# Performance work log

Measured on AMD Instinct MI355X. Metric: run time of the kernel, lower is better.

Reference implementation:

```python
import jax, jax.numpy as jnp
import numpy as np

B, N, D, H, DK, DI = 64, 256, 1024, 8, 64, 2048
NEG = -1e9
SCALE = 1.0 / np.sqrt(DK).astype(np.float32)


def _ln(x, s, b, eps=1e-5):
    m = jnp.mean(x, axis=-1, keepdims=True)
    v = jnp.var(x, axis=-1, keepdims=True)
    return (x - m) * jax.lax.rsqrt(v + eps) * s + b


def _glat_basic(x, mask, npm, wq, wk, wv, wo, bo, ls1, lb1, w1, b1, w2, b2, ls2, lb2):
    # mask: [B,1,N,N] bool, True = blocked
    b, n, d = x.shape
    q = (x @ wq).reshape(b, n, H, DK).transpose(0, 2, 1, 3)  # [B,H,N,DK]
    k = (x @ wk).reshape(b, n, H, DK).transpose(0, 2, 1, 3)
    v = (x @ wv).reshape(b, n, H, DK).transpose(0, 2, 1, 3)
    scores = jnp.einsum('bhqd,bhkd->bhqk', q, k) * SCALE
    scores = jnp.where(mask, NEG, scores)
    attn = jax.nn.softmax(scores, axis=-1)
    out = jnp.einsum('bhqk,bhkd->bhqd', attn, v)
    out = out.transpose(0, 2, 1, 3).reshape(b, n, H * DK)
    out = out @ wo + bo
    out = _ln(out + x, ls1, lb1)           # attn residual + layernorm
    out = out * npm                         # non_pad_mask
    h = jax.nn.relu(out @ w1 + b1) @ w2 + b2
    out2 = _ln(h + out, ls2, lb2) * npm     # FFN residual + layernorm + mask
    return out2


def setup_inputs():
    key = jax.random.key(0)
    ks = jax.random.split(key, 40)
    p = lambda i, shape: jax.random.normal(ks[i], shape, jnp.float32) * 0.02
    inp = {
        'x': jax.random.normal(ks[0], (B, N, D), jnp.float32),
        'adj': jax.random.randint(ks[1], (B, N, N), 0, 2).astype(jnp.int32),
        'non_pad_mask': jnp.ones((B, N, 1), jnp.float32),
        'slf_attn_mask': jnp.zeros((B, N, N), jnp.int32),
    }
    i = 2
    for t in ('g', 'l'):
        inp[f'wq_{t}'] = p(i, (D, H * DK)); i += 1
        inp[f'wk_{t}'] = p(i, (D, H * DK)); i += 1
        inp[f'wv_{t}'] = p(i, (D, H * DK)); i += 1
        inp[f'wo_{t}'] = p(i, (H * DK, D)); i += 1
        inp[f'bo_{t}'] = jnp.zeros((D,), jnp.float32)
        inp[f'ln1s_{t}'] = jnp.ones((D,), jnp.float32)
        inp[f'ln1b_{t}'] = jnp.zeros((D,), jnp.float32)
        inp[f'w1_{t}'] = p(i, (D, DI)); i += 1
        inp[f'b1_{t}'] = jnp.zeros((DI,), jnp.float32)
        inp[f'w2_{t}'] = p(i, (DI, D)); i += 1
        inp[f'b2_{t}'] = jnp.zeros((D,), jnp.float32)
        inp[f'ln2s_{t}'] = jnp.ones((D,), jnp.float32)
        inp[f'ln2b_{t}'] = jnp.zeros((D,), jnp.float32)
    inp['fc_w'] = p(i, (2 * D, D)); i += 1
    inp['fc_b'] = jnp.zeros((D,), jnp.float32)
    return inp


def reference(x, adj, non_pad_mask, slf_attn_mask,
              wq_g, wk_g, wv_g, wo_g, bo_g, ln1s_g, ln1b_g, w1_g, b1_g, w2_g, b2_g, ln2s_g, ln2b_g,
              wq_l, wk_l, wv_l, wo_l, bo_l, ln1s_l, ln1b_l, w1_l, b1_l, w2_l, b2_l, ln2s_l, ln2b_l,
              fc_w, fc_b):
    pad_mask = (slf_attn_mask[:, None, :, :] != 0)            # [B,1,N,N]
    local_mask = pad_mask | (adj[:, None, :, :] == 0)         # local: only attend along edges
    x_g = _glat_basic(x, pad_mask, non_pad_mask,
                      wq_g, wk_g, wv_g, wo_g, bo_g, ln1s_g, ln1b_g,
                      w1_g, b1_g, w2_g, b2_g, ln2s_g, ln2b_g)
    x_l = _glat_basic(x, local_mask, non_pad_mask,
                      wq_l, wk_l, wv_l, wo_l, bo_l, ln1s_l, ln1b_l,
                      w1_l, b1_l, w2_l, b2_l, ln2s_l, ln2b_l)
    out = jnp.concatenate([x_g, x_l], axis=-1) @ fc_w + fc_b
    return out
```

## Files before the change

### kernel.cpp

```cpp
#include <hip/hip_runtime.h>


typedef unsigned short u16;
typedef unsigned long long u64;
typedef __bf16 bf16_t;
typedef bf16_t bf16x8 __attribute__((ext_vector_type(8)));
typedef float  f32x4  __attribute__((ext_vector_type(4)));
typedef u16    u16x8  __attribute__((ext_vector_type(8)));
typedef u16    u16x4  __attribute__((ext_vector_type(4)));

__device__ __forceinline__ float bf2f(u16 u){
  union { unsigned int i; float f; } c; c.i = ((unsigned int)u) << 16; return c.f;
}
__device__ __forceinline__ u16 f2bf(float f){
  union { float f; unsigned int u; } c; c.f = f;
  unsigned int u = c.u;
  unsigned int r = (u + 0x7fffu + ((u >> 16) & 1u)) >> 16;
  return (u16)r;
}

__device__ __forceinline__ void gl16(const u16* g, u16* l){
  __builtin_amdgcn_global_load_lds(
      (const __attribute__((address_space(1))) void*)g,
      (__attribute__((address_space(3))) void*)l, 16, 0, 0);
}

__global__ __launch_bounds__(256) void zero_out(float* out, int n){
  for (int i = blockIdx.x * 256 + threadIdx.x; i < n; i += 256 * 4096) out[i] = 0.f;
}

__global__ __launch_bounds__(256) void cvt_bf16(
    const float* __restrict__ in, u16* __restrict__ out)
{
  const size_t i = ((size_t)blockIdx.x * 256 + threadIdx.x) * 8;
  f32x4 a = *(const f32x4*)&in[i];
  f32x4 b = *(const f32x4*)&in[i + 4];
  u16x8 o;
  #pragma unroll
  for (int j = 0; j < 4; ++j){ o[j] = f2bf(a[j]); o[4+j] = f2bf(b[j]); }
  *(u16x8*)&out[i] = o;
}

__global__ __launch_bounds__(256) void transpose_w(
    const float* __restrict__ src, u16* __restrict__ dst, int K, int N, int dstOff)
{
  __shared__ u16 tile[32][33];
  const int bk = blockIdx.x * 32, bn = blockIdx.y * 32;
  const int t = threadIdx.x;
  const int r = t >> 5, c = t & 31;
  #pragma unroll
  for (int p = 0; p < 4; ++p)
    tile[r + p*8][c] = f2bf(src[(size_t)(bk + r + p*8) * N + bn + c]);
  __syncthreads();
  #pragma unroll
  for (int p = 0; p < 4; ++p)
    dst[(size_t)(dstOff + bn + r + p*8) * K + bk + c] = tile[c][r + p*8];
}

__global__ __launch_bounds__(256) void transpose_qkv6(
    const float* s0, const float* s1, const float* s2,
    const float* s3, const float* s4, const float* s5,
    u16* __restrict__ dst0, u16* __restrict__ dst1)
{
  __shared__ u16 tile[32][33];
  const int z = blockIdx.z;
  const float* src = z == 0 ? s0 : z == 1 ? s1 : z == 2 ? s2
                   : z == 3 ? s3 : z == 4 ? s4 : s5;
  u16* dst = (z < 3 ? dst0 : dst1);
  const int dstOff = (z % 3) * 512;
  const int K = 1024, N = 512;
  const int bk = blockIdx.x * 32, bn = blockIdx.y * 32;
  const int t = threadIdx.x;
  const int r = t >> 5, c = t & 31;
  #pragma unroll
  for (int p = 0; p < 4; ++p)
    tile[r + p*8][c] = f2bf(src[(size_t)(bk + r + p*8) * N + bn + c]);
  __syncthreads();
  #pragma unroll
  for (int p = 0; p < 4; ++p)
    dst[(size_t)(dstOff + bn + r + p*8) * K + bk + c] = tile[c][r + p*8];
}

__global__ __launch_bounds__(256) void transpose_wo2(
    const float* s0, const float* s1, u16* __restrict__ dst0, u16* __restrict__ dst1)
{
  __shared__ u16 tile[32][33];
  const float* src = blockIdx.z == 0 ? s0 : s1;
  u16* dst = blockIdx.z == 0 ? dst0 : dst1;
  const int K = 512, N = 1024;
  const int bk = blockIdx.x * 32, bn = blockIdx.y * 32;
  const int t = threadIdx.x;
  const int r = t >> 5, c = t & 31;
  #pragma unroll
  for (int p = 0; p < 4; ++p)
    tile[r + p*8][c] = f2bf(src[(size_t)(bk + r + p*8) * N + bn + c]);
  __syncthreads();
  #pragma unroll
  for (int p = 0; p < 4; ++p)
    dst[(size_t)(bn + r + p*8) * K + bk + c] = tile[c][r + p*8];
}

template<int RELU, int OF32, int ACC, int OUT2>
__global__ __launch_bounds__(512, 1) void gemm256(
    const u16* __restrict__ A0, const u16* __restrict__ A1,
    int Astride, int ksplit,
    const u16* __restrict__ BT, int Bld, int M, int N, int K,
    const float* __restrict__ bias, void* __restrict__ outv, int out_ld,
    u16* __restrict__ out2v, int ncut)
{
  __shared__ u16 lds[2*32768];
  const int tid  = threadIdx.x;
  const int lane = tid & 63;
  const int wid  = tid >> 6;
  const int wm = wid >> 2, wn = wid & 3;
  const int l15 = lane & 15, l4 = lane >> 4;
  const int m0 = blockIdx.x * 256, n0 = blockIdx.y * 256;

  f32x4 acc[8][4];
  #pragma unroll
  for (int i = 0; i < 8; ++i)
    #pragma unroll
    for (int j = 0; j < 4; ++j)
      acc[i][j] = (f32x4){0.f, 0.f, 0.f, 0.f};

  const int s0 = tid, s1 = tid + 512;
  const int r0 = s0 >> 3, g0 = (s0 & 7) ^ (r0 & 7);
  const int r1 = s1 >> 3, g1 = (s1 & 7) ^ (r1 & 7);

  const int nt = K >> 6;

  auto stageA = [&](int kt, int h, int buf){
    const int kb = kt * 64;
    const u16* Ab = A0; int kl = kb;
    if (kb >= ksplit){ Ab = A1; kl = kb - ksplit; }
    u16* dst = &lds[buf*32768 + h*8192];
    gl16(&Ab[(size_t)(m0 + h*128 + r0) * Astride + kl + g0*8], &dst[s0*8]);
    gl16(&Ab[(size_t)(m0 + h*128 + r1) * Astride + kl + g1*8], &dst[s1*8]);
  };
  auto stageB = [&](int kt, int h, int buf){
    const int kb = kt * 64;
    u16* dst = &lds[buf*32768 + 16384 + h*8192];
    gl16(&BT[(size_t)(n0 + h*128 + r0) * Bld + kb + g0*8], &dst[s0*8]);
    gl16(&BT[(size_t)(n0 + h*128 + r1) * Bld + kb + g1*8], &dst[s1*8]);
  };
  auto lda = [&](int i, int kc, int buf) -> bf16x8 {
    const int r = wm*128 + i*16 + l15;
    const int c = (kc*4 + l4) ^ (r & 7);
    return *(const bf16x8*)&lds[buf*32768 + r*64 + c*8];
  };
  auto ldb = [&](int j, int kc, int buf) -> bf16x8 {
    const int r = wn*64 + j*16 + l15;
    const int c = (kc*4 + l4) ^ (r & 7);
    return *(const bf16x8*)&lds[buf*32768 + 16384 + r*64 + c*8];
  };

  stageA(0, 0, 0); stageA(0, 1, 0); stageB(0, 0, 0); stageB(0, 1, 0);

  for (int t = 0; t < nt; ++t){
    const int buf = t & 1, nbuf = buf ^ 1;
    const bool pf = (t + 1 < nt);
    if (pf){
      stageA(t+1, 0, nbuf);
      asm volatile("s_waitcnt vmcnt(2)" ::: "memory");
    } else {
      asm volatile("s_waitcnt vmcnt(0)" ::: "memory");
    }
    __builtin_amdgcn_sched_barrier(0);
    __builtin_amdgcn_s_barrier();
    __builtin_amdgcn_sched_barrier(0);

    bf16x8 a_[4][2], b_[2][2];
    #pragma unroll
    for (int i = 0; i < 4; ++i){ a_[i][0] = lda(i, 0, buf); a_[i][1] = lda(i, 1, buf); }
    #pragma unroll
    for (int j = 0; j < 2; ++j){ b_[j][0] = ldb(j, 0, buf); b_[j][1] = ldb(j, 1, buf); }
    if (pf) stageA(t+1, 1, nbuf);
    __builtin_amdgcn_s_setprio(1);
    #pragma unroll
    for (int i = 0; i < 4; ++i)
      #pragma unroll
      for (int j = 0; j < 2; ++j){
        acc[i][j] = __builtin_amdgcn_mfma_f32_16x16x32_bf16(a_[i][0], b_[j][0], acc[i][j], 0,0,0);
        acc[i][j] = __builtin_amdgcn_mfma_f32_16x16x32_bf16(a_[i][1], b_[j][1], acc[i][j], 0,0,0);
      }
    __builtin_amdgcn_s_setprio(0);
    #pragma unroll
    for (int j = 0; j < 2; ++j){ b_[j][0] = ldb(2+j, 0, buf); b_[j][1] = ldb(2+j, 1, buf); }
    if (pf) stageB(t+1, 0, nbuf);
    __builtin_amdgcn_s_setprio(1);
    #pragma unroll
    for (int i = 0; i < 4; ++i)
      #pragma unroll
      for (int j = 0; j < 2; ++j){
        acc[i][2+j] = __builtin_amdgcn_mfma_f32_16x16x32_bf16(a_[i][0], b_[j][0], acc[i][2+j], 0,0,0);
        acc[i][2+j] = __builtin_amdgcn_mfma_f32_16x16x32_bf16(a_[i][1], b_[j][1], acc[i][2+j], 0,0,0);
      }
    __builtin_amdgcn_s_setprio(0);
    #pragma unroll
    for (int i = 0; i < 4; ++i){ a_[i][0] = lda(4+i, 0, buf); a_[i][1] = lda(4+i, 1, buf); }
    if (pf) stageB(t+1, 1, nbuf);
    __builtin_amdgcn_s_setprio(1);
    #pragma unroll
    for (int i = 0; i < 4; ++i)
      #pragma unroll
      for (int j = 0; j < 2; ++j){
        acc[4+i][2+j] = __builtin_amdgcn_mfma_f32_16x16x32_bf16(a_[i][0], b_[j][0], acc[4+i][2+j], 0,0,0);
        acc[4+i][2+j] = __builtin_amdgcn_mfma_f32_16x16x32_bf16(a_[i][1], b_[j][1], acc[4+i][2+j], 0,0,0);
      }
    __builtin_amdgcn_s_setprio(0);
    #pragma unroll
    for (int j = 0; j < 2; ++j){ b_[j][0] = ldb(j, 0, buf); b_[j][1] = ldb(j, 1, buf); }
    __builtin_amdgcn_s_setprio(1);
    #pragma unroll
    for (int i = 0; i < 4; ++i)
      #pragma unroll
      for (int j = 0; j < 2; ++j){
        acc[4+i][j] = __builtin_amdgcn_mfma_f32_16x16x32_bf16(a_[i][0], b_[j][0], acc[4+i][j], 0,0,0);
        acc[4+i][j] = __builtin_amdgcn_mfma_f32_16x16x32_bf16(a_[i][1], b_[j][1], acc[4+i][j], 0,0,0);
      }
    __builtin_amdgcn_s_setprio(0);

    __builtin_amdgcn_sched_barrier(0);
    __builtin_amdgcn_s_barrier();
    __builtin_amdgcn_sched_barrier(0);
  }

  u16* outp = (u16*)outv;
  int cadj = 0;
  if (OUT2 && n0 >= ncut){ outp = out2v; cadj = ncut; }
  const int rb = m0 + wm*128 + l4*4;
  const int cb = n0 + wn*64 + l15;
  #pragma unroll
  for (int i = 0; i < 8; ++i){
    #pragma unroll
    for (int j = 0; j < 4; ++j){
      const int col = cb + j*16;
      const float badd = bias ? bias[col] : 0.f;
      #pragma unroll
      for (int r = 0; r < 4; ++r){
        const int row = rb + i*16 + r;
        float y = acc[i][j][r] + badd;
        if (RELU) y = y > 0.f ? y : 0.f;
        if (OF32){
          float* po = &((float*)outv)[(size_t)row * out_ld + col];
          if (ACC) y += *po;
          *po = y;
        } else {
          u16* po = &outp[(size_t)row * out_ld + col - cadj];
          if (ACC) y += bf2f(*po);
          *po = f2bf(y);
        }
      }
    }
  }
}

__global__ __launch_bounds__(256) void mask_pack(
    const int* __restrict__ slf, const int* __restrict__ adj,
    u64* __restrict__ mb_g, u64* __restrict__ mb_l)
{
  const int idx  = blockIdx.x * 4 + (threadIdx.x >> 6);
  const int lane = threadIdx.x & 63;
  const size_t mi = (size_t)(idx >> 2) * 256 + (size_t)(idx & 3) * 64 + lane;
  const bool g = slf[mi] != 0;
  const bool l = g || (adj[mi] == 0);
  const u64 bg = __ballot(g);
  const u64 bl = __ballot(l);
  if (lane == 0){ mb_g[idx] = bg; mb_l[idx] = bl; }
}

__global__ __launch_bounds__(256) void attn_mfma(
    const u16* __restrict__ qkv0, const u16* __restrict__ qkv1,
    const u64* __restrict__ mb0, const u64* __restrict__ mb1,
    u16* __restrict__ out0, u16* __restrict__ out1)
{
  __shared__ u16 kbuf[64*64];
  __shared__ u16 vtbuf[64*64];
  __shared__ u16 pbuf[4][32*64];

  const int L  = blockIdx.y;
  const u16* qkv = L ? qkv1 : qkv0;
  const u64* mb  = L ? mb1  : mb0;
  u16*       out = L ? out1 : out0;

  const int b  = blockIdx.x >> 4;
  const int h  = (blockIdx.x >> 1) & 7;
  const int qt = blockIdx.x & 1;
  const int t  = threadIdx.x;
  const int w  = t >> 6, lane = t & 63;
  const int l15 = lane & 15, l4 = lane >> 4;

  bf16x8 qf[2][2];
  {
    const int rbase = b*256 + qt*128 + w*32;
    #pragma unroll
    for (int i = 0; i < 2; ++i)
      #pragma unroll
      for (int kc = 0; kc < 2; ++kc)
        qf[i][kc] = *(const bf16x8*)&qkv[(size_t)(rbase + i*16 + l15)*1536 + h*64 + kc*32 + l4*8];
  }

  f32x4 acc_o[2][4];
  float m_[2][4], l_[2][4];
  #pragma unroll
  for (int i = 0; i < 2; ++i){
    #pragma unroll
    for (int j = 0; j < 4; ++j) acc_o[i][j] = (f32x4){0.f,0.f,0.f,0.f};
    #pragma unroll
    for (int r = 0; r < 4; ++r){ m_[i][r] = -1e30f; l_[i][r] = 0.f; }
  }

  for (int c = 0; c < 4; ++c){
    __syncthreads();
    {
      const int kr = t >> 2, dg = (t & 3) * 16;
      const size_t rbase = (size_t)(b*256 + c*64 + kr)*1536 + h*64 + dg;
      u16x8 k0 = *(const u16x8*)&qkv[rbase + 512];
      u16x8 k1 = *(const u16x8*)&qkv[rbase + 512 + 8];
      u16x8 v0 = *(const u16x8*)&qkv[rbase + 1024];
      u16x8 v1 = *(const u16x8*)&qkv[rbase + 1024 + 8];
      const int sw = (kr & 7) << 3;
      *(u16x8*)&kbuf[kr*64 + (dg ^ sw)]       = k0;
      *(u16x8*)&kbuf[kr*64 + ((dg + 8) ^ sw)] = k1;
      #pragma unroll
      for (int e = 0; e < 8; ++e){
        const int d0 = dg + e, d1 = dg + 8 + e;
        vtbuf[d0*64 + (kr ^ ((d0 & 7) << 3))] = v0[e];
        vtbuf[d1*64 + (kr ^ ((d1 & 7) << 3))] = v1[e];
      }
    }
    __syncthreads();

    bf16x8 kfr[4][2];
    #pragma unroll
    for (int jb = 0; jb < 4; ++jb){
      const int key = jb*16 + l15;
      const int sw = (key & 7) << 3;
      #pragma unroll
      for (int kc = 0; kc < 2; ++kc)
        kfr[jb][kc] = *(const bf16x8*)&kbuf[key*64 + ((kc*32 + l4*8) ^ sw)];
    }
    f32x4 s_[2][4];
    #pragma unroll
    for (int i = 0; i < 2; ++i)
      #pragma unroll
      for (int jb = 0; jb < 4; ++jb){
        f32x4 a = (f32x4){0.f,0.f,0.f,0.f};
        a = __builtin_amdgcn_mfma_f32_16x16x32_bf16(qf[i][0], kfr[jb][0], a, 0,0,0);
        a = __builtin_amdgcn_mfma_f32_16x16x32_bf16(qf[i][1], kfr[jb][1], a, 0,0,0);
        s_[i][jb] = a;
      }

    #pragma unroll
    for (int i = 0; i < 2; ++i)
      #pragma unroll
      for (int r = 0; r < 4; ++r){
        const int qrow = qt*128 + w*32 + i*16 + l4*4 + r;
        const u64 bits = mb[((size_t)b*256 + qrow)*4 + c];
        #pragma unroll
        for (int jb = 0; jb < 4; ++jb){
          float xv = s_[i][jb][r] * 0.125f;
          if ((bits >> (jb*16 + l15)) & 1ull) xv = -1e9f;
          s_[i][jb][r] = xv;
        }
      }
    float mxs[2][4];
    bool okall = true;
    #pragma unroll
    for (int i = 0; i < 2; ++i)
      #pragma unroll
      for (int r = 0; r < 4; ++r){
        float mx = fmaxf(fmaxf(s_[i][0][r], s_[i][1][r]),
                         fmaxf(s_[i][2][r], s_[i][3][r]));
        #pragma unroll
        for (int d = 1; d < 16; d <<= 1)
          mx = fmaxf(mx, __shfl_xor(mx, d, 64));
        mxs[i][r] = mx;
        okall = okall && (mx <= m_[i][r] + 8.f);
      }
    if (__all(okall)){
      #pragma unroll
      for (int i = 0; i < 2; ++i)
        #pragma unroll
        for (int r = 0; r < 4; ++r){
          const int prow = i*16 + l4*4 + r;
          const int swp = (prow & 7) << 3;
          float ps = 0.f;
          #pragma unroll
          for (int jb = 0; jb < 4; ++jb){
            const float p = __expf(s_[i][jb][r] - m_[i][r]);
            ps += p;
            pbuf[w][prow*64 + ((jb*16 + l15) ^ swp)] = f2bf(p);
          }
          #pragma unroll
          for (int d = 1; d < 16; d <<= 1)
            ps += __shfl_xor(ps, d, 64);
          l_[i][r] += ps;
        }
    } else {
      #pragma unroll
      for (int i = 0; i < 2; ++i)
        #pragma unroll
        for (int r = 0; r < 4; ++r){
          const int prow = i*16 + l4*4 + r;
          const float mnew = fmaxf(m_[i][r], mxs[i][r]);
          const float corr = __expf(m_[i][r] - mnew);
          m_[i][r] = mnew;
          float ps = 0.f;
          const int swp = (prow & 7) << 3;
          #pragma unroll
          for (int jb = 0; jb < 4; ++jb){
            const float p = __expf(s_[i][jb][r] - mnew);
            ps += p;
            pbuf[w][prow*64 + ((jb*16 + l15) ^ swp)] = f2bf(p);
          }
          #pragma unroll
          for (int d = 1; d < 16; d <<= 1)
            ps += __shfl_xor(ps, d, 64);
          l_[i][r] = l_[i][r] * corr + ps;
          #pragma unroll
          for (int j2 = 0; j2 < 4; ++j2) acc_o[i][j2][r] *= corr;
        }
    }

    bf16x8 vfr[4][2];
    #pragma unroll
    for (int j2 = 0; j2 < 4; ++j2){
      const int dim = j2*16 + l15;
      const int sw = (dim & 7) << 3;
      #pragma unroll
      for (int kc = 0; kc < 2; ++kc)
        vfr[j2][kc] = *(const bf16x8*)&vtbuf[dim*64 + ((kc*32 + l4*8) ^ sw)];
    }
    #pragma unroll
    for (int i = 0; i < 2; ++i){
      const int prow = i*16 + l15;
      const int swp = (prow & 7) << 3;
      bf16x8 pa0 = *(const bf16x8*)&pbuf[w][prow*64 + ((l4*8) ^ swp)];
      bf16x8 pa1 = *(const bf16x8*)&pbuf[w][prow*64 + ((32 + l4*8) ^ swp)];
      #pragma unroll
      for (int j2 = 0; j2 < 4; ++j2){
        acc_o[i][j2] = __builtin_amdgcn_mfma_f32_16x16x32_bf16(pa0, vfr[j2][0], acc_o[i][j2], 0,0,0);
        acc_o[i][j2] = __builtin_amdgcn_mfma_f32_16x16x32_bf16(pa1, vfr[j2][1], acc_o[i][j2], 0,0,0);
      }
    }
  }

  #pragma unroll
  for (int i = 0; i < 2; ++i){
    #pragma unroll
    for (int r = 0; r < 4; ++r){
      const int qrow = qt*128 + w*32 + i*16 + l4*4 + r;
      const float inv = 1.f / l_[i][r];
      const size_t ob = ((size_t)b*256 + qrow)*512 + h*64;
      #pragma unroll
      for (int j2 = 0; j2 < 4; ++j2)
        out[ob + j2*16 + l15] = f2bf(acc_o[i][j2][r] * inv);
    }
  }
}

template<int RF32>
__global__ __launch_bounds__(256) void ln_fused(
    const u16* a, const void* __restrict__ res,
    const float* __restrict__ sc, const float* __restrict__ bs,
    const float* __restrict__ npm, u16* out)
{
  const int w = threadIdx.x >> 6, lane = threadIdx.x & 63;
  const int row = blockIdx.x * 4 + w;
  const size_t bse = (size_t)row * 1024 + lane * 16;

  u16x8 av0 = *(const u16x8*)&a[bse];
  u16x8 av1 = *(const u16x8*)&a[bse + 8];
  float rv[16];
  if (RF32){
    const float* rp = (const float*)res + bse;
    #pragma unroll
    for (int j = 0; j < 16; j += 4){
      f32x4 q = *(const f32x4*)&rp[j];
      rv[j] = q[0]; rv[j+1] = q[1]; rv[j+2] = q[2]; rv[j+3] = q[3];
    }
  } else {
    const u16* rp = (const u16*)res + bse;
    u16x8 q0 = *(const u16x8*)rp;
    u16x8 q1 = *(const u16x8*)(rp + 8);
    #pragma unroll
    for (int j = 0; j < 8; ++j){ rv[j] = bf2f(q0[j]); rv[8+j] = bf2f(q1[j]); }
  }

  float vv[16]; float s = 0.f, sq = 0.f;
  #pragma unroll
  for (int j = 0; j < 8; ++j){
    vv[j]   = bf2f(av0[j]) + rv[j];
    vv[8+j] = bf2f(av1[j]) + rv[8+j];
  }
  #pragma unroll
  for (int j = 0; j < 16; ++j){ s += vv[j]; sq += vv[j]*vv[j]; }
  #pragma unroll
  for (int i = 1; i < 64; i <<= 1){
    s  += __shfl_xor(s,  i, 64);
    sq += __shfl_xor(sq, i, 64);
  }
  const float mean = s * (1.f/1024.f);
  const float var  = sq * (1.f/1024.f) - mean*mean;
  const float rstd = rsqrtf(var + 1e-5f);
  const float nm   = npm[row];

  u16x8 o0, o1;
  #pragma unroll
  for (int j = 0; j < 8; ++j){
    const int c0 = lane*16 + j, c1 = c0 + 8;
    o0[j] = f2bf(((vv[j]   - mean) * rstd * sc[c0] + bs[c0]) * nm);
    o1[j] = f2bf(((vv[8+j] - mean) * rstd * sc[c1] + bs[c1]) * nm);
  }
  *(u16x8*)&out[bse]     = o0;
  *(u16x8*)&out[bse + 8] = o1;
}

extern "C" void kernel_launch(void* const* d_in, const int* in_sizes, int n_in,
                              void* d_out, int out_size, void* d_ws, size_t ws_size,
                              hipStream_t stream)
{
  const size_t NEED = 58720256ull * 2ull;
  if (ws_size < NEED){
    zero_out<<<4096, 256, 0, stream>>>((float*)d_out, out_size);
    return;
  }

  const float* x   = (const float*)d_in[0];
  const int*   adj = (const int*)d_in[1];
  const float* npm = (const float*)d_in[2];
  const int*   slf = (const int*)d_in[3];
  const float* fcw = (const float*)d_in[30];
  const float* fcb = (const float*)d_in[31];

  u16* ws     = (u16*)d_ws;
  u16* wqkvT0 = ws;
  u16* wqkvT1 = ws + 1572864;
  u16* woT0   = ws + 3145728;
  u16* woT1   = ws + 3670016;
  u16* fcT    = ws + 4194304;
  u64* mb_g   = (u64*)(ws + 6291456);
  u64* mb_l   = mb_g + 65536;
  u16* w1T    = ws + 6291456;
  u16* w2T    = ws;
  u16* xbf    = ws + 8388608;
  u16* tmp0   = ws + 8388608;
  u16* qkv1   = ws + 25165824;
  u16* ln1    = ws + 25165824;
  u16* tmp1   = ws + 41943040;
  u16* attnb0 = ws + 50331648;

  u16* dout16 = (u16*)d_out;
  u16* qkv0   = dout16;
  u16* attnb1 = dout16 + 25165824;
  u16* hbuf   = dout16;

  cvt_bf16<<<8192, 256, 0, stream>>>(x, xbf);
  mask_pack<<<16384, 256, 0, stream>>>(slf, adj, mb_g, mb_l);
  transpose_w<<<dim3(64, 32), 256, 0, stream>>>(fcw, fcT, 2048, 1024, 0);
  transpose_qkv6<<<dim3(32, 16, 6), 256, 0, stream>>>(
      (const float*)d_in[4+0], (const float*)d_in[4+1], (const float*)d_in[4+2],
      (const float*)d_in[17+0], (const float*)d_in[17+1], (const float*)d_in[17+2],
      wqkvT0, wqkvT1);
  transpose_wo2<<<dim3(16, 32, 2), 256, 0, stream>>>(
      (const float*)d_in[4+3], (const float*)d_in[17+3], woT0, woT1);

  gemm256<0,0,0,1><<<dim3(64, 12), 512, 0, stream>>>(
      xbf, xbf, 1024, 1024, wqkvT0, 1024, 16384, 3072, 1024,
      nullptr, qkv0, 1536, qkv1, 1536);
  attn_mfma<<<dim3(1024, 2), 256, 0, stream>>>(
      qkv0, qkv1, mb_g, mb_l, attnb0, attnb1);

  gemm256<0,0,0,0><<<dim3(64, 4), 512, 0, stream>>>(
      attnb0, attnb0, 512, 512, woT0, 512, 16384, 1024, 512,
      (const float*)d_in[4+4], tmp0, 1024, nullptr, 0);
  gemm256<0,0,0,0><<<dim3(64, 4), 512, 0, stream>>>(
      attnb1, attnb1, 512, 512, woT1, 512, 16384, 1024, 512,
      (const float*)d_in[17+4], tmp1, 1024, nullptr, 0);

  for (int L = 0; L < 2; ++L){
    const int bi = 4 + L*13;
    const float* l1s = (const float*)d_in[bi+5];
    const float* l1b = (const float*)d_in[bi+6];
    const float* b1  = (const float*)d_in[bi+8];
    const float* b2  = (const float*)d_in[bi+10];
    const float* l2s = (const float*)d_in[bi+11];
    const float* l2b = (const float*)d_in[bi+12];
    u16* tmpL = L ? tmp1 : tmp0;

    transpose_w<<<dim3(32, 64), 256, 0, stream>>>((const float*)d_in[bi+7], w1T, 1024, 2048, 0);
    transpose_w<<<dim3(64, 32), 256, 0, stream>>>((const float*)d_in[bi+9], w2T, 2048, 1024, 0);

    ln_fused<1><<<4096, 256, 0, stream>>>(tmpL, x, l1s, l1b, npm, ln1);
    gemm256<1,0,0,0><<<dim3(64, 8), 512, 0, stream>>>(
        ln1, ln1, 1024, 1024, w1T, 1024, 16384, 2048, 1024, b1, hbuf, 2048,
        nullptr, 0);
    gemm256<0,0,0,0><<<dim3(64, 4), 512, 0, stream>>>(
        hbuf, hbuf, 2048, 2048, w2T, 2048, 16384, 1024, 2048, b2, tmpL, 1024,
        nullptr, 0);
    ln_fused<0><<<4096, 256, 0, stream>>>(tmpL, ln1, l2s, l2b, npm, tmpL);
  }

  gemm256<0,1,0,0><<<dim3(64, 4), 512, 0, stream>>>(
      tmp0, tmp1, 1024, 1024, fcT, 2048, 16384, 1024, 2048, fcb, d_out, 1024,
      nullptr, 0);
}
```

Before: 683.7 us.

## Merge both Wo projections into one GEMM launch, batch weight transposes, keep B fragments

Result: no change. 677.0 us (-1.0%).

```diff
diff --git a/kernel.cpp b/kernel.cpp
--- a/kernel.cpp
+++ b/kernel.cpp
@@ -55,6 +55,25 @@
   #pragma unroll
   for (int p = 0; p < 4; ++p)
     dst[(size_t)(dstOff + bn + r + p*8) * K + bk + c] = tile[c][r + p*8];
+}
+
+__global__ __launch_bounds__(256) void transpose_w2(
+    const float* s0, const float* s1, u16* __restrict__ d0, u16* __restrict__ d1,
+    int K, int N)
+{
+  __shared__ u16 tile[32][33];
+  const float* src = blockIdx.z == 0 ? s0 : s1;
+  u16* dst = blockIdx.z == 0 ? d0 : d1;
+  const int bk = blockIdx.x * 32, bn = blockIdx.y * 32;
+  const int t = threadIdx.x;
+  const int r = t >> 5, c = t & 31;
+  #pragma unroll
+  for (int p = 0; p < 4; ++p)
+    tile[r + p*8][c] = f2bf(src[(size_t)(bk + r + p*8) * N + bn + c]);
+  __syncthreads();
+  #pragma unroll
+  for (int p = 0; p < 4; ++p)
+    dst[(size_t)(bn + r + p*8) * K + bk + c] = tile[c][r + p*8];
 }
 
 __global__ __launch_bounds__(256) void transpose_qkv6(
@@ -81,32 +100,13 @@
     dst[(size_t)(dstOff + bn + r + p*8) * K + bk + c] = tile[c][r + p*8];
 }
 
-__global__ __launch_bounds__(256) void transpose_wo2(
-    const float* s0, const float* s1, u16* __restrict__ dst0, u16* __restrict__ dst1)
-{
-  __shared__ u16 tile[32][33];
-  const float* src = blockIdx.z == 0 ? s0 : s1;
-  u16* dst = blockIdx.z == 0 ? dst0 : dst1;
-  const int K = 512, N = 1024;
-  const int bk = blockIdx.x * 32, bn = blockIdx.y * 32;
-  const int t = threadIdx.x;
-  const int r = t >> 5, c = t & 31;
-  #pragma unroll
-  for (int p = 0; p < 4; ++p)
-    tile[r + p*8][c] = f2bf(src[(size_t)(bk + r + p*8) * N + bn + c]);
-  __syncthreads();
-  #pragma unroll
-  for (int p = 0; p < 4; ++p)
-    dst[(size_t)(bn + r + p*8) * K + bk + c] = tile[c][r + p*8];
-}
-
-template<int RELU, int OF32, int ACC, int OUT2>
+template<int RELU, int OF32, int ACC, int OUT2, int NSPLIT>
 __global__ __launch_bounds__(512, 1) void gemm256(
     const u16* __restrict__ A0, const u16* __restrict__ A1,
     int Astride, int ksplit,
     const u16* __restrict__ BT, int Bld, int M, int N, int K,
     const float* __restrict__ bias, void* __restrict__ outv, int out_ld,
-    u16* __restrict__ out2v, int ncut)
+    u16* __restrict__ out2v, const float* __restrict__ bias2, int ncut)
 {
   __shared__ u16 lds[2*32768];
   const int tid  = threadIdx.x;
@@ -116,6 +116,9 @@
   const int l15 = lane & 15, l4 = lane >> 4;
   const int m0 = blockIdx.x * 256, n0 = blockIdx.y * 256;
 
+  const bool hi = (OUT2 || NSPLIT) && (n0 >= ncut);
+  const u16* Aeff = (NSPLIT && hi) ? A1 : A0;
+
   f32x4 acc[8][4];
   #pragma unroll
   for (int i = 0; i < 8; ++i)
@@ -131,8 +134,8 @@
 
   auto stageA = [&](int kt, int h, int buf){
     const int kb = kt * 64;
-    const u16* Ab = A0; int kl = kb;
-    if (kb >= ksplit){ Ab = A1; kl = kb - ksplit; }
+    const u16* Ab = Aeff; int kl = kb;
+    if (!NSPLIT && kb >= ksplit){ Ab = A1; kl = kb - ksplit; }
     u16* dst = &lds[buf*32768 + h*8192];
     gl16(&Ab[(size_t)(m0 + h*128 + r0) * Astride + kl + g0*8], &dst[s0*8]);
     gl16(&Ab[(size_t)(m0 + h*128 + r1) * Astride + kl + g1*8], &dst[s1*8]);
@@ -169,11 +172,11 @@
     __builtin_amdgcn_s_barrier();
     __builtin_amdgcn_sched_barrier(0);
 
-    bf16x8 a_[4][2], b_[2][2];
+    bf16x8 a_[4][2], b_[4][2];
+    #pragma unroll
+    for (int j = 0; j < 4; ++j){ b_[j][0] = ldb(j, 0, buf); b_[j][1] = ldb(j, 1, buf); }
     #pragma unroll
     for (int i = 0; i < 4; ++i){ a_[i][0] = lda(i, 0, buf); a_[i][1] = lda(i, 1, buf); }
-    #pragma unroll
-    for (int j = 0; j < 2; ++j){ b_[j][0] = ldb(j, 0, buf); b_[j][1] = ldb(j, 1, buf); }
     if (pf) stageA(t+1, 1, nbuf);
     __builtin_amdgcn_s_setprio(1);
     #pragma unroll
@@ -184,16 +187,14 @@
         acc[i][j] = __builtin_amdgcn_mfma_f32_16x16x32_bf16(a_[i][1], b_[j][1], acc[i][j], 0,0,0);
       }
     __builtin_amdgcn_s_setprio(0);
-    #pragma unroll
-    for (int j = 0; j < 2; ++j){ b_[j][0] = ldb(2+j, 0, buf); b_[j][1] = ldb(2+j, 1, buf); }
     if (pf) stageB(t+1, 0, nbuf);
     __builtin_amdgcn_s_setprio(1);
     #pragma unroll
     for (int i = 0; i < 4; ++i)
       #pragma unroll
       for (int j = 0; j < 2; ++j){
-        acc[i][2+j] = __builtin_amdgcn_mfma_f32_16x16x32_bf16(a_[i][0], b_[j][0], acc[i][2+j], 0,0,0);
-        acc[i][2+j] = __builtin_amdgcn_mfma_f32_16x16x32_bf16(a_[i][1], b_[j][1], acc[i][2+j], 0,0,0);
+        acc[i][2+j] = __builtin_amdgcn_mfma_f32_16x16x32_bf16(a_[i][0], b_[2+j][0], acc[i][2+j], 0,0,0);
+        acc[i][2+j] = __builtin_amdgcn_mfma_f32_16x16x32_bf16(a_[i][1], b_[2+j][1], acc[i][2+j], 0,0,0);
       }
     __builtin_amdgcn_s_setprio(0);
     #pragma unroll
@@ -204,12 +205,10 @@
     for (int i = 0; i < 4; ++i)
       #pragma unroll
       for (int j = 0; j < 2; ++j){
-        acc[4+i][2+j] = __builtin_amdgcn_mfma_f32_16x16x32_bf16(a_[i][0], b_[j][0], acc[4+i][2+j], 0,0,0);
-        acc[4+i][2+j] = __builtin_amdgcn_mfma_f32_16x16x32_bf16(a_[i][1], b_[j][1], acc[4+i][2+j], 0,0,0);
+        acc[4+i][2+j] = __builtin_amdgcn_mfma_f32_16x16x32_bf16(a_[i][0], b_[2+j][0], acc[4+i][2+j], 0,0,0);
+        acc[4+i][2+j] = __builtin_amdgcn_mfma_f32_16x16x32_bf16(a_[i][1], b_[2+j][1], acc[4+i][2+j], 0,0,0);
       }
     __builtin_amdgcn_s_setprio(0);
-    #pragma unroll
-    for (int j = 0; j < 2; ++j){ b_[j][0] = ldb(j, 0, buf); b_[j][1] = ldb(j, 1, buf); }
     __builtin_amdgcn_s_setprio(1);
     #pragma unroll
     for (int i = 0; i < 4; ++i)
@@ -226,8 +225,9 @@
   }
 
   u16* outp = (u16*)outv;
+  const float* bp = bias;
   int cadj = 0;
-  if (OUT2 && n0 >= ncut){ outp = out2v; cadj = ncut; }
+  if (hi){ outp = out2v; bp = NSPLIT ? bias2 : bias; cadj = ncut; }
   const int rb = m0 + wm*128 + l4*4;
   const int cb = n0 + wn*64 + l15;
   #pragma unroll
@@ -235,7 +235,7 @@
     #pragma unroll
     for (int j = 0; j < 4; ++j){
       const int col = cb + j*16;
-      const float badd = bias ? bias[col] : 0.f;
+      const float badd = bp ? bp[col - cadj] : 0.f;
       #pragma unroll
       for (int r = 0; r < 4; ++r){
         const int row = rb + i*16 + r;
@@ -539,11 +539,13 @@
   u16* wqkvT1 = ws + 1572864;
   u16* woT0   = ws + 3145728;
   u16* woT1   = ws + 3670016;
-  u16* fcT    = ws + 4194304;
   u64* mb_g   = (u64*)(ws + 6291456);
   u64* mb_l   = mb_g + 65536;
-  u16* w1T    = ws + 6291456;
-  u16* w2T    = ws;
+  u16* w1T0   = ws;
+  u16* w1T1   = ws + 2097152;
+  u16* w2T0   = ws + 4194304;
+  u16* w2T1   = ws + 6291456;
+  u16* fcT    = ws;
   u16* xbf    = ws + 8388608;
   u16* tmp0   = ws + 8388608;
   u16* qkv1   = ws + 25165824;
@@ -558,26 +560,27 @@
 
   cvt_bf16<<<8192, 256, 0, stream>>>(x, xbf);
   mask_pack<<<16384, 256, 0, stream>>>(slf, adj, mb_g, mb_l);
-  transpose_w<<<dim3(64, 32), 256, 0, stream>>>(fcw, fcT, 2048, 1024, 0);
   transpose_qkv6<<<dim3(32, 16, 6), 256, 0, stream>>>(
       (const float*)d_in[4+0], (const float*)d_in[4+1], (const float*)d_in[4+2],
       (const float*)d_in[17+0], (const float*)d_in[17+1], (const float*)d_in[17+2],
       wqkvT0, wqkvT1);
-  transpose_wo2<<<dim3(16, 32, 2), 256, 0, stream>>>(
-      (const float*)d_in[4+3], (const float*)d_in[17+3], woT0, woT1);
-
-  gemm256<0,0,0,1><<<dim3(64, 12), 512, 0, stream>>>(
+  transpose_w2<<<dim3(16, 32, 2), 256, 0, stream>>>(
+      (const float*)d_in[4+3], (const float*)d_in[17+3], woT0, woT1, 512, 1024);
+
+  gemm256<0,0,0,1,0><<<dim3(64, 12), 512, 0, stream>>>(
       xbf, xbf, 1024, 1024, wqkvT0, 1024, 16384, 3072, 1024,
-      nullptr, qkv0, 1536, qkv1, 1536);
+      nullptr, qkv0, 1536, qkv1, nullptr, 1536);
   attn_mfma<<<dim3(1024, 2), 256, 0, stream>>>(
       qkv0, qkv1, mb_g, mb_l, attnb0, attnb1);
 
-  gemm256<0,0,0,0><<<dim3(64, 4), 512, 0, stream>>>(
-      attnb0, attnb0, 512, 512, woT0, 512, 16384, 1024, 512,
-      (const float*)d_in[4+4], tmp0, 1024, nullptr, 0);
-  gemm256<0,0,0,0><<<dim3(64, 4), 512, 0, stream>>>(
-      attnb1, attnb1, 512, 512, woT1, 512, 16384, 1024, 512,
-      (const float*)d_in[17+4], tmp1, 1024, nullptr, 0);
+  gemm256<0,0,0,0,1><<<dim3(64, 8), 512, 0, stream>>>(
+      attnb0, attnb1, 512, 512, woT0, 512, 16384, 2048, 512,
+      (const float*)d_in[4+4], tmp0, 1024, tmp1, (const float*)d_in[17+4], 1024);
+
+  transpose_w2<<<dim3(32, 64, 2), 256, 0, stream>>>(
+      (const float*)d_in[4+7], (const float*)d_in[17+7], w1T0, w1T1, 1024, 2048);
+  transpose_w2<<<dim3(64, 32, 2), 256, 0, stream>>>(
+      (const float*)d_in[4+9], (const float*)d_in[17+9], w2T0, w2T1, 2048, 1024);
 
   for (int L = 0; L < 2; ++L){
     const int bi = 4 + L*13;
@@ -588,21 +591,21 @@
     const float* l2s = (const float*)d_in[bi+11];
     const float* l2b = (const float*)d_in[bi+12];
     u16* tmpL = L ? tmp1 : tmp0;
-
-    transpose_w<<<dim3(32, 64), 256, 0, stream>>>((const float*)d_in[bi+7], w1T, 1024, 2048, 0);
-    transpose_w<<<dim3(64, 32), 256, 0, stream>>>((const float*)d_in[bi+9], w2T, 2048, 1024, 0);
+    u16* w1TL = L ? w1T1 : w1T0;
+    u16* w2TL = L ? w2T1 : w2T0;
 
     ln_fused<1><<<4096, 256, 0, stream>>>(tmpL, x, l1s, l1b, npm, ln1);
-    gemm256<1,0,0,0><<<dim3(64, 8), 512, 0, stream>>>(
-        ln1, ln1, 1024, 1024, w1T, 1024, 16384, 2048, 1024, b1, hbuf, 2048,
-        nullptr, 0);
-    gemm256<0,0,0,0><<<dim3(64, 4), 512, 0, stream>>>(
-        hbuf, hbuf, 2048, 2048, w2T, 2048, 16384, 1024, 2048, b2, tmpL, 1024,
-        nullptr, 0);
+    gemm256<1,0,0,0,0><<<dim3(64, 8), 512, 0, stream>>>(
+        ln1, ln1, 1024, 1024, w1TL, 1024, 16384, 2048, 1024, b1, hbuf, 2048,
+        nullptr, nullptr, 0);
+    gemm256<0,0,0,0,0><<<dim3(64, 4), 512, 0, stream>>>(
+        hbuf, hbuf, 2048, 2048, w2TL, 2048, 16384, 1024, 2048, b2, tmpL, 1024,
+        nullptr, nullptr, 0);
     ln_fused<0><<<4096, 256, 0, stream>>>(tmpL, ln1, l2s, l2b, npm, tmpL);
   }
 
-  gemm256<0,1,0,0><<<dim3(64, 4), 512, 0, stream>>>(
+  transpose_w<<<dim3(64, 32), 256, 0, stream>>>(fcw, fcT, 2048, 1024, 0);
+  gemm256<0,1,0,0,0><<<dim3(64, 4), 512, 0, stream>>>(
       tmp0, tmp1, 1024, 1024, fcT, 2048, 16384, 1024, 2048, fcb, d_out, 1024,
-      nullptr, 0);
-}
+      nullptr, nullptr, 0);
+}
```
